# Performance work log

Measured on AMD Instinct MI355X. Metric: run time of the kernel, lower is better.

Reference implementation:

```python
import jax, jax.numpy as jnp
import numpy as np

NCHARS = 50000
NWORDS = 500000
NIC = 64      # ninput_char
NIW = 64      # ninput_word
NH = 128      # nhidden
NA = 5        # naction (nmapping_fn)
B = 65536     # batch size


def setup_inputs() -> dict:
    key = jax.random.key(0)
    ks = jax.random.split(key, 12)
    s = 0.05
    return {
        "x": jax.random.randint(ks[0], (B, 2), 0, NCHARS),
        "y": jax.random.randint(ks[1], (B,), 0, NWORDS),
        "cemb_table": jax.random.normal(ks[2], (NCHARS, NIC), jnp.float32) * s,
        "wemb_table": jax.random.normal(ks[3], (NWORDS, NIW), jnp.float32) * s,
        # Policy MLP: Linear(2*NIC -> NH), ReLU, Linear(NH -> NA), Softmax
        "Wp1": jax.random.normal(ks[4], (2 * NIC, NH), jnp.float32) * s,
        "bp1": jnp.zeros((NH,), jnp.float32),
        "Wp2": jax.random.normal(ks[5], (NH, NA), jnp.float32) * s,
        "bp2": jnp.zeros((NA,), jnp.float32),
        # NA expert MLPs, stacked: Linear(2*NIC -> NH), ReLU, Linear(NH -> NIW)
        "We1": jax.random.normal(ks[6], (NA, 2 * NIC, NH), jnp.float32) * s,
        "be1": jnp.zeros((NA, NH), jnp.float32),
        "We2": jax.random.normal(ks[7], (NA, NH, NIW), jnp.float32) * s,
        "be2": jnp.zeros((NA, NIW), jnp.float32),
    }


def reference(x, y, cemb_table, wemb_table, Wp1, bp1, Wp2, bp2, We1, be1, We2, be2):
    bsize = x.shape[0]
    # char_embs(x).view(bsize, -1): [B, 2*NIC]
    cembs = cemb_table[x].reshape(bsize, -1)

    # Policy (dropout off in eval): probs = softmax(relu(cembs@Wp1+bp1)@Wp2+bp2)
    # Categorical sampling over probs == categorical over the pre-softmax logits.
    logits = jnp.maximum(cembs @ Wp1 + bp1, 0.0) @ Wp2 + bp2
    action = jax.random.categorical(jax.random.key(42), logits)   # [B]
    action_mask = jax.nn.one_hot(action, NA, dtype=cembs.dtype)   # [B, NA]

    # Dense evaluation of all NA experts (matches the Python loop + stack)
    h = jnp.maximum(jnp.einsum('bd,adh->bah', cembs, We1) + be1, 0.0)  # [B, NA, NH]
    mapped = jnp.einsum('bah,aho->bao', h, We2) + be2                  # [B, NA, NIW]

    # sum(unsqueeze(mask,-1) * mapped, dim=1)
    out = jnp.einsum('ba,bao->bo', action_mask, mapped)               # [B, NIW]

    wemb = wemb_table[y]                                              # [B, NIW]
    return (out, wemb)
```

## Files before the change

### kernel.cpp

```cpp
#include <hip/hip_runtime.h>
#include <stdint.h>

#define B_N   65536
#define NIC   64
#define NIW   64
#define NH    128
#define NA    5
#define D2    128

#define PARTITIONABLE 1

#define P2_NCHUNK 51
#define P2_R      1286

typedef __attribute__((ext_vector_type(8))) short short8;
typedef __attribute__((ext_vector_type(4))) float f32x4;

__device__ __forceinline__ ushort f2bf(float f) {
  uint32_t u = __float_as_uint(f);
  uint32_t r = (u + 0x7FFFu + ((u >> 16) & 1u)) >> 16;
  return (ushort)r;
}

__device__ __forceinline__ void split2(float f, ushort& h, ushort& l) {
  h = f2bf(f);
  l = f2bf(f - __uint_as_float(((uint32_t)h) << 16));
}

__device__ __forceinline__ void threefry2x32_k042(uint32_t x0, uint32_t x1,
                                                  uint32_t& o0, uint32_t& o1) {
  const uint32_t ks0 = 0u;
  const uint32_t ks1 = 42u;
  const uint32_t ks2 = 0x1BD11BDAu ^ 0u ^ 42u;
  x0 += ks0; x1 += ks1;
#define TF_RND(r) { x0 += x1; x1 = (x1 << (r)) | (x1 >> (32 - (r))); x1 ^= x0; }
  TF_RND(13) TF_RND(15) TF_RND(26) TF_RND(6)
  x0 += ks1; x1 += ks2 + 1u;
  TF_RND(17) TF_RND(29) TF_RND(16) TF_RND(24)
  x0 += ks2; x1 += ks0 + 2u;
  TF_RND(13) TF_RND(15) TF_RND(26) TF_RND(6)
  x0 += ks0; x1 += ks1 + 3u;
  TF_RND(17) TF_RND(29) TF_RND(16) TF_RND(24)
  x0 += ks1; x1 += ks2 + 4u;
  TF_RND(13) TF_RND(15) TF_RND(26) TF_RND(6)
  x0 += ks2; x1 += ks0 + 5u;
#undef TF_RND
  o0 = x0; o1 = x1;
}

__device__ __forceinline__ float gumbel_at(uint32_t idx) {
  uint32_t bits;
#if PARTITIONABLE
  uint32_t a, b;
  threefry2x32_k042(0u, idx, a, b);
  bits = a ^ b;
#else
  const uint32_t HALF = (uint32_t)(B_N * NA) / 2u;
  uint32_t a, b;
  if (idx < HALF) { threefry2x32_k042(idx, idx + HALF, a, b); bits = a; }
  else            { threefry2x32_k042(idx - HALF, idx, a, b); bits = b; }
#endif
  const float f = __uint_as_float((bits >> 9) | 0x3f800000u) - 1.0f;
  const double u = (f == 0.0f) ? (double)0x1p-126 : (double)f;
  const float nl = (float)(-log(u));
  const float g  = (float)(-log((double)nl));
  return g;
}

__global__ __launch_bounds__(512, 1) void policy_kernel(
    const int* __restrict__ x, const int* __restrict__ y,
    const float* __restrict__ cemb, const float* __restrict__ wemb,
    const float* __restrict__ Wp1, const float* __restrict__ bp1,
    const float* __restrict__ Wp2, const float* __restrict__ bp2,
    float* __restrict__ out_wemb, int* __restrict__ action) {
  __shared__ __align__(16) ushort sW1h[32 * 512];
  __shared__ __align__(16) ushort sW1l[32 * 512];
  __shared__ __align__(16) float sCH[128][132];
  __shared__ __align__(16) float sW2t[NA][NH];
  __shared__ __align__(16) float sb1[NH];
  __shared__ __align__(16) float sScore[128][6];

  const int tid = threadIdx.x;
  const int base = blockIdx.x * 128;

  {
    const int n = tid & 127, q = tid >> 7;
    const int fb = (n >> 4) * 4 + q;
    const int c16 = n & 15;
#pragma unroll
    for (int grp = 0; grp < 4; grp++) {
      short8 ph, pl;
#pragma unroll
      for (int j = 0; j < 8; j++) {
        const int k = 32 * q + 8 * grp + j;
        ushort hh, ll;
        split2(Wp1[k * NH + n], hh, ll);
        ph[j] = (short)hh;
        pl[j] = (short)ll;
      }
      *(short8*)&sW1h[fb * 512 + (c16 + 16 * grp) * 8] = ph;
      *(short8*)&sW1l[fb * 512 + (c16 + 16 * grp) * 8] = pl;
    }
    if (tid < NH) sb1[tid] = bp1[tid];
    if (tid < NA * 32) {
      const int a = tid >> 5, k0 = (tid & 31) * 4;
#pragma unroll
      for (int j = 0; j < 4; j++) sW2t[a][k0 + j] = Wp2[(k0 + j) * NA + a];
    }
  }

  const int wave = tid >> 6, lane = tid & 63;
  const int c16 = lane & 15, h2 = lane >> 4;

  const int grow = base + wave * 16 + c16;
  const int xi0 = x[grow * 2], xi1 = x[grow * 2 + 1];
  short8 Ah[4], Al[4];
#pragma unroll
  for (int kt = 0; kt < 4; kt++) {
    const int xi = (kt < 2) ? xi0 : xi1;
    const float* src = cemb + (size_t)xi * NIC + (kt & 1) * 32 + h2 * 8;
    const float4 aa = *(const float4*)src;
    const float4 bb = *(const float4*)(src + 4);
    ushort hh, ll;
    short8 ph, pl;
    split2(aa.x, hh, ll); ph[0] = (short)hh; pl[0] = (short)ll;
    split2(aa.y, hh, ll); ph[1] = (short)hh; pl[1] = (short)ll;
    split2(aa.z, hh, ll); ph[2] = (short)hh; pl[2] = (short)ll;
    split2(aa.w, hh, ll); ph[3] = (short)hh; pl[3] = (short)ll;
    split2(bb.x, hh, ll); ph[4] = (short)hh; pl[4] = (short)ll;
    split2(bb.y, hh, ll); ph[5] = (short)hh; pl[5] = (short)ll;
    split2(bb.z, hh, ll); ph[6] = (short)hh; pl[6] = (short)ll;
    split2(bb.w, hh, ll); ph[7] = (short)hh; pl[7] = (short)ll;
    Ah[kt] = ph;
    Al[kt] = pl;
  }
  __syncthreads();

  f32x4 acc[8];
#pragma unroll
  for (int ct = 0; ct < 8; ct++) {
    const float bv = sb1[ct * 16 + c16];
    acc[ct] = (f32x4){bv, bv, bv, bv};
  }
#pragma unroll
  for (int kt = 0; kt < 4; kt++) {
#pragma unroll
    for (int ct = 0; ct < 8; ct++) {
      const short8 Bh = *(const short8*)&sW1h[(ct * 4 + kt) * 512 + lane * 8];
      const short8 Bl = *(const short8*)&sW1l[(ct * 4 + kt) * 512 + lane * 8];
      acc[ct] = __builtin_amdgcn_mfma_f32_16x16x32_bf16(Ah[kt], Bh, acc[ct], 0, 0, 0);
      acc[ct] = __builtin_amdgcn_mfma_f32_16x16x32_bf16(Al[kt], Bh, acc[ct], 0, 0, 0);
      acc[ct] = __builtin_amdgcn_mfma_f32_16x16x32_bf16(Ah[kt], Bl, acc[ct], 0, 0, 0);
      acc[ct] = __builtin_amdgcn_mfma_f32_16x16x32_bf16(Al[kt], Bl, acc[ct], 0, 0, 0);
    }
  }
  {
    const int rowb = wave * 16 + h2 * 4;
#pragma unroll
    for (int ct = 0; ct < 8; ct++) {
      const int n = ct * 16 + c16;
#pragma unroll
      for (int r = 0; r < 4; r++)
        sCH[rowb + r][n] = fmaxf(acc[ct][r], 0.0f);
    }
  }
  __syncthreads();

#pragma unroll 1
  for (int p = tid; p < 128 * NA; p += 512) {
    const int row = p / NA, a = p - NA * row;
    float s0 = 0.f, s1 = 0.f, s2 = 0.f, s3 = 0.f;
#pragma unroll 4
    for (int k = 0; k < NH; k += 4) {
      const float4 h4 = *(const float4*)&sCH[row][k];
      const float4 w4 = *(const float4*)&sW2t[a][k];
      s0 = fmaf(h4.x, w4.x, s0);
      s1 = fmaf(h4.y, w4.y, s1);
      s2 = fmaf(h4.z, w4.z, s2);
      s3 = fmaf(h4.w, w4.w, s3);
    }
    const float logit = ((s0 + s1) + (s2 + s3)) + bp2[a];
    sScore[row][a] = gumbel_at((uint32_t)((base + row) * NA + a)) + logit;
  }
  __syncthreads();

  if (tid < 128) {
    int best = 0;
    float bs = sScore[tid][0];
#pragma unroll
    for (int a = 1; a < NA; a++) {
      const float s = sScore[tid][a];
      if (s > bs) { bs = s; best = a; }
    }
    action[base + tid] = best;
  }

#pragma unroll 1
  for (int i = tid; i < 128 * 16; i += 512) {
    const int row = i >> 4, seg = i & 15;
    ((float4*)out_wemb)[(size_t)(base + row) * 16 + seg] =
        ((const float4*)wemb)[(size_t)y[base + row] * 16 + seg];
  }
}

__global__ __launch_bounds__(512, 1) void expert_kernel(
    const int* __restrict__ x, const float* __restrict__ cemb,
    const float* __restrict__ We1, const float* __restrict__ be1,
    const float* __restrict__ We2, const float* __restrict__ be2,
    const int* __restrict__ action, float* __restrict__ out) {
  __shared__ __align__(16) ushort sW1[32 * 512];
  __shared__ __align__(16) ushort sW2[16 * 512];
  __shared__ __align__(16) ushort sCt[8][4 * 512];
  __shared__ __align__(16) ushort sHt[8][4 * 512];
  __shared__ __align__(16) float sbe1[NH];
  __shared__ __align__(16) float sbe2[NIW];
  __shared__ int sList[P2_R];
  __shared__ int sCount;

  const int tid = threadIdx.x;
  const int a = blockIdx.x % NA;
  const int chunk = blockIdx.x / NA;
  const int rowBeg = chunk * P2_R;
  const int rowEnd = (rowBeg + P2_R < B_N) ? rowBeg + P2_R : B_N;

  if (tid == 0) sCount = 0;
  __syncthreads();

  for (int r = rowBeg + tid; r < rowEnd; r += 512)
    if (action[r] == a) sList[atomicAdd(&sCount, 1)] = r;

  {
    const float* W1g = We1 + (size_t)a * D2 * NH;
    const int n = tid & 127, q = tid >> 7;
    const int fb = (n >> 4) * 4 + q;
    const int c16 = n & 15;
#pragma unroll
    for (int grp = 0; grp < 4; grp++) {
      short8 pk;
#pragma unroll
      for (int j = 0; j < 8; j++) {
        const int k = 32 * q + 8 * grp + j;
        pk[j] = (short)f2bf(W1g[k * NH + n]);
      }
      *(short8*)&sW1[fb * 512 + (c16 + 16 * grp) * 8] = pk;
    }
    if (tid < NH) sbe1[tid] = be1[a * NH + tid];
    if (tid < NIW) sbe2[tid] = be2[a * NIW + tid];
  }
  {
    const float* W2g = We2 + (size_t)a * NH * NIW;
    const int o = tid & 63, hq = tid >> 6;
    const int fb = (o >> 4) * 4 + (hq >> 1);
    const int c16 = o & 15;
#pragma unroll
    for (int g2 = 0; g2 < 2; g2++) {
      const int grp = (hq & 1) * 2 + g2;
      short8 pk;
#pragma unroll
      for (int j = 0; j < 8; j++) {
        const int h = 16 * hq + 8 * g2 + j;
        pk[j] = (short)f2bf(W2g[h * NIW + o]);
      }
      *(short8*)&sW2[fb * 512 + (c16 + 16 * grp) * 8] = pk;
    }
  }
  __syncthreads();

  const int cnt = sCount;
  if (cnt == 0) return;

  const int wave = tid >> 6, lane = tid & 63;
  const int rowb = (lane >> 4) * 4;
  ushort* myCt = sCt[wave];
  ushort* myHt = sHt[wave];

#pragma unroll 1
  for (int t16 = wave * 16; t16 < cnt; t16 += 128) {
    {
      const int rt = lane >> 2, q = lane & 3;
      int li = t16 + rt;
      const int g = sList[(li < cnt) ? li : 0];
      const int xi = x[2 * g + (q >> 1)];
      const float4* src = (const float4*)(cemb + (size_t)xi * NIC + (q & 1) * 32);
#pragma unroll
      for (int grp = 0; grp < 4; grp++) {
        const float4 aa = src[2 * grp], bb = src[2 * grp + 1];
        short8 pk;
        pk[0] = (short)f2bf(aa.x); pk[1] = (short)f2bf(aa.y);
        pk[2] = (short)f2bf(aa.z); pk[3] = (short)f2bf(aa.w);
        pk[4] = (short)f2bf(bb.x); pk[5] = (short)f2bf(bb.y);
        pk[6] = (short)f2bf(bb.z); pk[7] = (short)f2bf(bb.w);
        *(short8*)&myCt[q * 512 + (rt + 16 * grp) * 8] = pk;
      }
    }

    short8 A[4];
#pragma unroll
    for (int kt = 0; kt < 4; kt++) A[kt] = *(const short8*)&myCt[kt * 512 + lane * 8];
#pragma unroll
    for (int ct = 0; ct < 8; ct++) {
      const int n = ct * 16 + (lane & 15);
      const float bv = sbe1[n];
      f32x4 acc = {bv, bv, bv, bv};
#pragma unroll
      for (int kt = 0; kt < 4; kt++) {
        const short8 Bf = *(const short8*)&sW1[(ct * 4 + kt) * 512 + lane * 8];
        acc = __builtin_amdgcn_mfma_f32_16x16x32_bf16(A[kt], Bf, acc, 0, 0, 0);
      }
      const int kt2 = n >> 5, grp2 = (n & 31) >> 3, j2 = n & 7;
#pragma unroll
      for (int r = 0; r < 4; r++) {
        const float hv = fmaxf(acc[r], 0.0f);
        myHt[kt2 * 512 + ((rowb + r) + 16 * grp2) * 8 + j2] = f2bf(hv);
      }
    }

    short8 A2[4];
#pragma unroll
    for (int kt = 0; kt < 4; kt++) A2[kt] = *(const short8*)&myHt[kt * 512 + lane * 8];
    int gr4[4];
#pragma unroll
    for (int r = 0; r < 4; r++) {
      const int li2 = t16 + rowb + r;
      gr4[r] = (li2 < cnt) ? sList[li2] : -1;
    }
#pragma unroll
    for (int ot = 0; ot < 4; ot++) {
      const int o = ot * 16 + (lane & 15);
      const float bv = sbe2[o];
      f32x4 o4 = {bv, bv, bv, bv};
#pragma unroll
      for (int kt = 0; kt < 4; kt++) {
        const short8 Bf = *(const short8*)&sW2[(ot * 4 + kt) * 512 + lane * 8];
        o4 = __builtin_amdgcn_mfma_f32_16x16x32_bf16(A2[kt], Bf, o4, 0, 0, 0);
      }
#pragma unroll
      for (int r = 0; r < 4; r++) {
        if (gr4[r] >= 0) out[(size_t)gr4[r] * NIW + o] = o4[r];
      }
    }
  }
}

extern "C" void kernel_launch(void* const* d_in, const int* in_sizes, int n_in,
                              void* d_out, int out_size, void* d_ws, size_t ws_size,
                              hipStream_t stream) {
  const int*   x    = (const int*)d_in[0];
  const int*   y    = (const int*)d_in[1];
  const float* cemb = (const float*)d_in[2];
  const float* wemb = (const float*)d_in[3];
  const float* Wp1  = (const float*)d_in[4];
  const float* bp1  = (const float*)d_in[5];
  const float* Wp2  = (const float*)d_in[6];
  const float* bp2  = (const float*)d_in[7];
  const float* We1  = (const float*)d_in[8];
  const float* be1  = (const float*)d_in[9];
  const float* We2  = (const float*)d_in[10];
  const float* be2  = (const float*)d_in[11];

  float* out      = (float*)d_out;
  float* out_wemb = out + (size_t)B_N * NIW;
  int*   action   = (int*)d_ws;

  policy_kernel<<<B_N / 128, 512, 0, stream>>>(
      x, y, cemb, wemb, Wp1, bp1, Wp2, bp2, out_wemb, action);
  expert_kernel<<<NA * P2_NCHUNK, 512, 0, stream>>>(
      x, cemb, We1, be1, We2, be2, action, out);
}
```

Baseline: 50.73 us.

## Prepack expert weights in policy launch and gather experts per 128-row block

Five extra blocks in the policy kernel convert the expert weights to bf16 MFMA layout once and store them in the workspace. A new expert kernel then reads those packed weights straight from global memory, so it no longer stages them in LDS. Each block groups its own 128 rows by action and runs 16-row tiles for every expert, with higher occupancy. The policy GEMM also drops the lo*lo split-bf16 MFMA term, trading a little logit precision for fewer MFMAs, which could flip sampled actions near ties.

```diff
diff --git a/kernel.cpp b/kernel.cpp
--- a/kernel.cpp
+++ b/kernel.cpp
@@ -10,8 +10,14 @@
 
 #define PARTITIONABLE 1
 
+#define NBLK  512
+
 #define P2_NCHUNK 51
 #define P2_R      1286
+
+#define WS_ACTION_BYTES  262144
+#define WS_PREP_BYTES    245760
+#define WS_NEED_FAST     (WS_ACTION_BYTES + WS_PREP_BYTES)
 
 typedef __attribute__((ext_vector_type(8))) short short8;
 typedef __attribute__((ext_vector_type(4))) float f32x4;
@@ -72,7 +78,9 @@
     const float* __restrict__ cemb, const float* __restrict__ wemb,
     const float* __restrict__ Wp1, const float* __restrict__ bp1,
     const float* __restrict__ Wp2, const float* __restrict__ bp2,
-    float* __restrict__ out_wemb, int* __restrict__ action) {
+    const float* __restrict__ We1, const float* __restrict__ We2,
+    float* __restrict__ out_wemb, int* __restrict__ action,
+    ushort* __restrict__ wPrep) {
   __shared__ __align__(16) ushort sW1h[32 * 512];
   __shared__ __align__(16) ushort sW1l[32 * 512];
   __shared__ __align__(16) float sCH[128][132];
@@ -81,12 +89,48 @@
   __shared__ __align__(16) float sScore[128][6];
 
   const int tid = threadIdx.x;
+
+  if (blockIdx.x >= NBLK) {
+    const int a = blockIdx.x - NBLK;
+    ushort* wp = wPrep + (size_t)a * 24576;
+    {
+      const float* W1g = We1 + (size_t)a * D2 * NH;
+      const int n = tid & 127, q = tid >> 7;
+      const int fb = (n >> 4) * 4 + q;
+      const int cc = n & 15;
+#pragma unroll
+      for (int grp = 0; grp < 4; grp++) {
+        short8 pk;
+#pragma unroll
+        for (int j = 0; j < 8; j++)
+          pk[j] = (short)f2bf(W1g[(32 * q + 8 * grp + j) * NH + n]);
+        *(short8*)&wp[fb * 512 + (cc + 16 * grp) * 8] = pk;
+      }
+    }
+    {
+      const float* W2g = We2 + (size_t)a * NH * NIW;
+      const int o = tid & 63, hq = tid >> 6;
+      const int fb = (o >> 4) * 4 + (hq >> 1);
+      const int cc = o & 15;
+#pragma unroll
+      for (int g2 = 0; g2 < 2; g2++) {
+        const int grp = (hq & 1) * 2 + g2;
+        short8 pk;
+#pragma unroll
+        for (int j = 0; j < 8; j++)
+          pk[j] = (short)f2bf(W2g[(16 * hq + 8 * g2 + j) * NIW + o]);
+        *(short8*)&wp[16384 + fb * 512 + (cc + 16 * grp) * 8] = pk;
+      }
+    }
+    return;
+  }
+
   const int base = blockIdx.x * 128;
 
   {
     const int n = tid & 127, q = tid >> 7;
     const int fb = (n >> 4) * 4 + q;
-    const int c16 = n & 15;
+    const int cc = n & 15;
 #pragma unroll
     for (int grp = 0; grp < 4; grp++) {
       short8 ph, pl;
@@ -98,8 +142,8 @@
         ph[j] = (short)hh;
         pl[j] = (short)ll;
       }
-      *(short8*)&sW1h[fb * 512 + (c16 + 16 * grp) * 8] = ph;
-      *(short8*)&sW1l[fb * 512 + (c16 + 16 * grp) * 8] = pl;
+      *(short8*)&sW1h[fb * 512 + (cc + 16 * grp) * 8] = ph;
+      *(short8*)&sW1l[fb * 512 + (cc + 16 * grp) * 8] = pl;
     }
     if (tid < NH) sb1[tid] = bp1[tid];
     if (tid < NA * 32) {
@@ -151,7 +195,6 @@
       acc[ct] = __builtin_amdgcn_mfma_f32_16x16x32_bf16(Ah[kt], Bh, acc[ct], 0, 0, 0);
       acc[ct] = __builtin_amdgcn_mfma_f32_16x16x32_bf16(Al[kt], Bh, acc[ct], 0, 0, 0);
       acc[ct] = __builtin_amdgcn_mfma_f32_16x16x32_bf16(Ah[kt], Bl, acc[ct], 0, 0, 0);
-      acc[ct] = __builtin_amdgcn_mfma_f32_16x16x32_bf16(Al[kt], Bl, acc[ct], 0, 0, 0);
     }
   }
   {
@@ -203,7 +246,117 @@
   }
 }
 
-__global__ __launch_bounds__(512, 1) void expert_kernel(
+__global__ __launch_bounds__(512, 4) void expert_prepacked(
+    const int* __restrict__ x, const float* __restrict__ cemb,
+    const float* __restrict__ be1, const float* __restrict__ be2,
+    const int* __restrict__ action, const ushort* __restrict__ wPrep,
+    float* __restrict__ out) {
+  __shared__ __align__(16) ushort sHt[8][2048];
+  __shared__ int sList[NA][128];
+  __shared__ int sCnt[NA];
+  __shared__ __align__(16) float sbe1f[NA * NH];
+  __shared__ __align__(16) float sbe2f[NA * NIW];
+
+  const int tid = threadIdx.x;
+  const int base = blockIdx.x * 128;
+
+  if (tid < NA) sCnt[tid] = 0;
+  __syncthreads();
+  if (tid < 128) {
+    const int a = action[base + tid];
+    const int p = atomicAdd(&sCnt[a], 1);
+    sList[a][p] = base + tid;
+  }
+  for (int i = tid; i < NA * NH; i += 512) sbe1f[i] = be1[i];
+  for (int i = tid; i < NA * NIW; i += 512) sbe2f[i] = be2[i];
+  __syncthreads();
+
+  int cnts[NA], pre[NA + 1];
+  pre[0] = 0;
+#pragma unroll
+  for (int a = 0; a < NA; a++) {
+    cnts[a] = sCnt[a];
+    pre[a + 1] = pre[a] + ((cnts[a] + 15) >> 4);
+  }
+  const int T = pre[NA];
+
+  const int wave = tid >> 6, lane = tid & 63;
+  const int c16 = lane & 15, h2 = lane >> 4;
+  const int rowb = h2 * 4;
+  ushort* myHt = sHt[wave];
+
+#pragma unroll 1
+  for (int t = wave; t < T; t += 8) {
+    int a = 0;
+#pragma unroll
+    for (int q = 1; q < NA; q++) if (t >= pre[q]) a = q;
+    const int ti = t - pre[a];
+    const int cnt = cnts[a];
+    const ushort* wp1 = wPrep + (size_t)a * 24576;
+    const ushort* wp2 = wp1 + 16384;
+
+    const int slot = ti * 16 + c16;
+    const int g = sList[a][(slot < cnt) ? slot : 0];
+    const int2 xi2 = ((const int2*)x)[g];
+    short8 Ah[4];
+#pragma unroll
+    for (int kt = 0; kt < 4; kt++) {
+      const float* src = cemb + (size_t)((kt < 2) ? xi2.x : xi2.y) * NIC +
+                         (kt & 1) * 32 + h2 * 8;
+      const float4 aa = *(const float4*)src;
+      const float4 bb = *(const float4*)(src + 4);
+      short8 pk;
+      pk[0] = (short)f2bf(aa.x); pk[1] = (short)f2bf(aa.y);
+      pk[2] = (short)f2bf(aa.z); pk[3] = (short)f2bf(aa.w);
+      pk[4] = (short)f2bf(bb.x); pk[5] = (short)f2bf(bb.y);
+      pk[6] = (short)f2bf(bb.z); pk[7] = (short)f2bf(bb.w);
+      Ah[kt] = pk;
+    }
+
+#pragma unroll
+    for (int ct = 0; ct < 8; ct++) {
+      const float bv = sbe1f[a * NH + ct * 16 + c16];
+      f32x4 acc = {bv, bv, bv, bv};
+#pragma unroll
+      for (int kt = 0; kt < 4; kt++) {
+        const short8 Bf = *(const short8*)&wp1[(ct * 4 + kt) * 512 + lane * 8];
+        acc = __builtin_amdgcn_mfma_f32_16x16x32_bf16(Ah[kt], Bf, acc, 0, 0, 0);
+      }
+      const int n = ct * 16 + c16;
+      const int kt2 = n >> 5, grp2 = (n & 31) >> 3, j2 = n & 7;
+#pragma unroll
+      for (int r = 0; r < 4; r++)
+        myHt[kt2 * 512 + ((rowb + r) + 16 * grp2) * 8 + j2] =
+            f2bf(fmaxf(acc[r], 0.0f));
+    }
+
+    short8 A2[4];
+#pragma unroll
+    for (int kt = 0; kt < 4; kt++)
+      A2[kt] = *(const short8*)&myHt[kt * 512 + lane * 8];
+    int gr4[4];
+#pragma unroll
+    for (int r = 0; r < 4; r++) {
+      const int li2 = ti * 16 + rowb + r;
+      gr4[r] = (li2 < cnt) ? sList[a][li2] : -1;
+    }
+#pragma unroll
+    for (int ot = 0; ot < 4; ot++) {
+      const float bv = sbe2f[a * NIW + ot * 16 + c16];
+      f32x4 o4 = {bv, bv, bv, bv};
+#pragma unroll
+      for (int kt = 0; kt < 4; kt++) {
+        const short8 Bf = *(const short8*)&wp2[(ot * 4 + kt) * 512 + lane * 8];
+        o4 = __builtin_amdgcn_mfma_f32_16x16x32_bf16(A2[kt], Bf, o4, 0, 0, 0);
+      }
+#pragma unroll
+      for (int r = 0; r < 4; r++)
+        if (gr4[r] >= 0) out[(size_t)gr4[r] * NIW + ot * 16 + c16] = o4[r];
+    }
+  }
+}
+
+__global__ __launch_bounds__(512, 1) void expert_staged(
     const int* __restrict__ x, const float* __restrict__ cemb,
     const float* __restrict__ We1, const float* __restrict__ be1,
     const float* __restrict__ We2, const float* __restrict__ be2,
@@ -233,16 +386,14 @@
     const float* W1g = We1 + (size_t)a * D2 * NH;
     const int n = tid & 127, q = tid >> 7;
     const int fb = (n >> 4) * 4 + q;
-    const int c16 = n & 15;
+    const int cc = n & 15;
 #pragma unroll
     for (int grp = 0; grp < 4; grp++) {
       short8 pk;
 #pragma unroll
-      for (int j = 0; j < 8; j++) {
-        const int k = 32 * q + 8 * grp + j;
-        pk[j] = (short)f2bf(W1g[k * NH + n]);
-      }
-      *(short8*)&sW1[fb * 512 + (c16 + 16 * grp) * 8] = pk;
+      for (int j = 0; j < 8; j++)
+        pk[j] = (short)f2bf(W1g[(32 * q + 8 * grp + j) * NH + n]);
+      *(short8*)&sW1[fb * 512 + (cc + 16 * grp) * 8] = pk;
     }
     if (tid < NH) sbe1[tid] = be1[a * NH + tid];
     if (tid < NIW) sbe2[tid] = be2[a * NIW + tid];
@@ -251,17 +402,15 @@
     const float* W2g = We2 + (size_t)a * NH * NIW;
     const int o = tid & 63, hq = tid >> 6;
     const int fb = (o >> 4) * 4 + (hq >> 1);
-    const int c16 = o & 15;
+    const int cc = o & 15;
 #pragma unroll
     for (int g2 = 0; g2 < 2; g2++) {
       const int grp = (hq & 1) * 2 + g2;
       short8 pk;
 #pragma unroll
-      for (int j = 0; j < 8; j++) {
-        const int h = 16 * hq + 8 * g2 + j;
-        pk[j] = (short)f2bf(W2g[h * NIW + o]);
-      }
-      *(short8*)&sW2[fb * 512 + (c16 + 16 * grp) * 8] = pk;
+      for (int j = 0; j < 8; j++)
+        pk[j] = (short)f2bf(W2g[(16 * hq + 8 * g2 + j) * NIW + o]);
+      *(short8*)&sW2[fb * 512 + (cc + 16 * grp) * 8] = pk;
     }
   }
   __syncthreads();
@@ -309,10 +458,9 @@
       }
       const int kt2 = n >> 5, grp2 = (n & 31) >> 3, j2 = n & 7;
 #pragma unroll
-      for (int r = 0; r < 4; r++) {
-        const float hv = fmaxf(acc[r], 0.0f);
-        myHt[kt2 * 512 + ((rowb + r) + 16 * grp2) * 8 + j2] = f2bf(hv);
-      }
+      for (int r = 0; r < 4; r++)
+        myHt[kt2 * 512 + ((rowb + r) + 16 * grp2) * 8 + j2] =
+            f2bf(fmaxf(acc[r], 0.0f));
     }
 
     short8 A2[4];
@@ -335,9 +483,8 @@
         o4 = __builtin_amdgcn_mfma_f32_16x16x32_bf16(A2[kt], Bf, o4, 0, 0, 0);
       }
 #pragma unroll
-      for (int r = 0; r < 4; r++) {
+      for (int r = 0; r < 4; r++)
         if (gr4[r] >= 0) out[(size_t)gr4[r] * NIW + o] = o4[r];
-      }
     }
   }
 }
@@ -360,10 +507,20 @@
 
   float* out      = (float*)d_out;
   float* out_wemb = out + (size_t)B_N * NIW;
-  int*   action   = (int*)d_ws;
-
-  policy_kernel<<<B_N / 128, 512, 0, stream>>>(
-      x, y, cemb, wemb, Wp1, bp1, Wp2, bp2, out_wemb, action);
-  expert_kernel<<<NA * P2_NCHUNK, 512, 0, stream>>>(
-      x, cemb, We1, be1, We2, be2, action, out);
-}
+  int*    action  = (int*)d_ws;
+  ushort* wPrep   = (ushort*)((char*)d_ws + WS_ACTION_BYTES);
+
+  const bool fast = (ws_size >= (size_t)WS_NEED_FAST);
+
+  if (fast) {
+    policy_kernel<<<NBLK + NA, 512, 0, stream>>>(
+        x, y, cemb, wemb, Wp1, bp1, Wp2, bp2, We1, We2, out_wemb, action, wPrep);
+    expert_prepacked<<<NBLK, 512, 0, stream>>>(
+        x, cemb, be1, be2, action, wPrep, out);
+  } else {
+    policy_kernel<<<NBLK, 512, 0, stream>>>(
+        x, y, cemb, wemb, Wp1, bp1, Wp2, bp2, We1, We2, out_wemb, action, wPrep);
+    expert_staged<<<NA * P2_NCHUNK, 512, 0, stream>>>(
+        x, cemb, We1, be1, We2, be2, action, out);
+  }
+}
```

After: 59.62 us. 17.5% more time.

## Fuse policy and expert kernels with per-block action bucketing and prepacked weights

Applied to the files above, without the earlier changes.

Merges the policy and expert passes into one kernel: each block computes actions for its 128 rows, buckets the rows by action in shared memory, and runs the expert MLPs on those rows while reusing the bf16 char-embedding fragments kept in LDS. A small prepack kernel converts the expert weights to bf16 MFMA layout once, and the fused kernel reads them from global/L2 instead of loading them per block. It also drops the low*low correction MFMA in the policy GEMM. This removes the action round-trip, the second launch and the second embedding gather, at the cost of expert weights being streamed from L2 on every tile and slightly lower precision in the policy logits, which could flip sampled actions.

```diff
diff --git a/kernel.cpp b/kernel.cpp
--- a/kernel.cpp
+++ b/kernel.cpp
@@ -10,8 +10,7 @@
 
 #define PARTITIONABLE 1
 
-#define P2_NCHUNK 51
-#define P2_R      1286
+#define NBLK  512
 
 typedef __attribute__((ext_vector_type(8))) short short8;
 typedef __attribute__((ext_vector_type(4))) float f32x4;
@@ -67,18 +66,61 @@
   return g;
 }
 
-__global__ __launch_bounds__(512, 1) void policy_kernel(
+__global__ __launch_bounds__(512, 1) void prepack_kernel(
+    const float* __restrict__ We1, const float* __restrict__ We2,
+    ushort* __restrict__ wPrep) {
+  const int tid = threadIdx.x;
+  const int a = blockIdx.x;
+  ushort* wp = wPrep + (size_t)a * 24576;
+  {
+    const float* W1g = We1 + (size_t)a * D2 * NH;
+    const int n = tid & 127, q = tid >> 7;
+    const int fb = (n >> 4) * 4 + q;
+    const int cc = n & 15;
+#pragma unroll
+    for (int grp = 0; grp < 4; grp++) {
+      short8 pk;
+#pragma unroll
+      for (int j = 0; j < 8; j++)
+        pk[j] = (short)f2bf(W1g[(32 * q + 8 * grp + j) * NH + n]);
+      *(short8*)&wp[fb * 512 + (cc + 16 * grp) * 8] = pk;
+    }
+  }
+  {
+    const float* W2g = We2 + (size_t)a * NH * NIW;
+    const int o = tid & 63, hq = tid >> 6;
+    const int fb = (o >> 4) * 4 + (hq >> 1);
+    const int cc = o & 15;
+#pragma unroll
+    for (int g2 = 0; g2 < 2; g2++) {
+      const int grp = (hq & 1) * 2 + g2;
+      short8 pk;
+#pragma unroll
+      for (int j = 0; j < 8; j++)
+        pk[j] = (short)f2bf(W2g[(16 * hq + 8 * g2 + j) * NIW + o]);
+      *(short8*)&wp[16384 + fb * 512 + (cc + 16 * grp) * 8] = pk;
+    }
+  }
+}
+
+__global__ __launch_bounds__(512, 1) void fused_kernel(
     const int* __restrict__ x, const int* __restrict__ y,
     const float* __restrict__ cemb, const float* __restrict__ wemb,
     const float* __restrict__ Wp1, const float* __restrict__ bp1,
     const float* __restrict__ Wp2, const float* __restrict__ bp2,
-    float* __restrict__ out_wemb, int* __restrict__ action) {
-  __shared__ __align__(16) ushort sW1h[32 * 512];
-  __shared__ __align__(16) ushort sW1l[32 * 512];
+    const float* __restrict__ be1, const float* __restrict__ be2,
+    const ushort* __restrict__ wPrep,
+    float* __restrict__ out, float* __restrict__ out_wemb) {
+  __shared__ __align__(16) ushort sW1h[16384];
+  __shared__ __align__(16) ushort sW1l[16384];
   __shared__ __align__(16) float sCH[128][132];
   __shared__ __align__(16) float sW2t[NA][NH];
   __shared__ __align__(16) float sb1[NH];
   __shared__ __align__(16) float sScore[128][6];
+  __shared__ __align__(16) float sbe1f[NA * NH];
+  __shared__ __align__(16) float sbe2f[NA * NIW];
+  __shared__ int sList[NA][128];
+  __shared__ int sCnt[NA];
 
   const int tid = threadIdx.x;
   const int base = blockIdx.x * 128;
@@ -86,7 +128,7 @@
   {
     const int n = tid & 127, q = tid >> 7;
     const int fb = (n >> 4) * 4 + q;
-    const int c16 = n & 15;
+    const int cc = n & 15;
 #pragma unroll
     for (int grp = 0; grp < 4; grp++) {
       short8 ph, pl;
@@ -98,8 +140,8 @@
         ph[j] = (short)hh;
         pl[j] = (short)ll;
       }
-      *(short8*)&sW1h[fb * 512 + (c16 + 16 * grp) * 8] = ph;
-      *(short8*)&sW1l[fb * 512 + (c16 + 16 * grp) * 8] = pl;
+      *(short8*)&sW1h[fb * 512 + (cc + 16 * grp) * 8] = ph;
+      *(short8*)&sW1l[fb * 512 + (cc + 16 * grp) * 8] = pl;
     }
     if (tid < NH) sb1[tid] = bp1[tid];
     if (tid < NA * 32) {
@@ -107,12 +149,23 @@
 #pragma unroll
       for (int j = 0; j < 4; j++) sW2t[a][k0 + j] = Wp2[(k0 + j) * NA + a];
     }
+    if (tid < NA) sCnt[tid] = 0;
+  }
+  for (int i = tid; i < NA * NH; i += 512) sbe1f[i] = be1[i];
+  for (int i = tid; i < NA * NIW; i += 512) sbe2f[i] = be2[i];
+
+#pragma unroll 1
+  for (int i = tid; i < 128 * 16; i += 512) {
+    const int row = i >> 4, seg = i & 15;
+    ((float4*)out_wemb)[(size_t)(base + row) * 16 + seg] =
+        ((const float4*)wemb)[(size_t)y[base + row] * 16 + seg];
   }
 
   const int wave = tid >> 6, lane = tid & 63;
   const int c16 = lane & 15, h2 = lane >> 4;
 
-  const int grow = base + wave * 16 + c16;
+  const int rloc = wave * 16 + c16;
+  const int grow = base + rloc;
   const int xi0 = x[grow * 2], xi1 = x[grow * 2 + 1];
   short8 Ah[4], Al[4];
 #pragma unroll
@@ -151,9 +204,11 @@
       acc[ct] = __builtin_amdgcn_mfma_f32_16x16x32_bf16(Ah[kt], Bh, acc[ct], 0, 0, 0);
       acc[ct] = __builtin_amdgcn_mfma_f32_16x16x32_bf16(Al[kt], Bh, acc[ct], 0, 0, 0);
       acc[ct] = __builtin_amdgcn_mfma_f32_16x16x32_bf16(Ah[kt], Bl, acc[ct], 0, 0, 0);
-      acc[ct] = __builtin_amdgcn_mfma_f32_16x16x32_bf16(Al[kt], Bl, acc[ct], 0, 0, 0);
-    }
-  }
+    }
+  }
+  __syncthreads();
+
+  ushort* sAf = sW1h;
   {
     const int rowb = wave * 16 + h2 * 4;
 #pragma unroll
@@ -162,6 +217,11 @@
 #pragma unroll
       for (int r = 0; r < 4; r++)
         sCH[rowb + r][n] = fmaxf(acc[ct][r], 0.0f);
+    }
+#pragma unroll
+    for (int kt = 0; kt < 4; kt++) {
+      const int cs = (kt * 4 + h2 + rloc) & 15;
+      *(short8*)&sAf[rloc * 128 + cs * 8] = Ah[kt];
     }
   }
   __syncthreads();
@@ -192,152 +252,80 @@
       const float s = sScore[tid][a];
       if (s > bs) { bs = s; best = a; }
     }
-    action[base + tid] = best;
-  }
+    const int p = atomicAdd(&sCnt[best], 1);
+    sList[best][p] = tid;
+  }
+  __syncthreads();
+
+  const int c0 = sCnt[0], c1 = sCnt[1], c2 = sCnt[2], c3 = sCnt[3], c4 = sCnt[4];
+  const int p1 = (c0 + 15) >> 4;
+  const int p2 = p1 + ((c1 + 15) >> 4);
+  const int p3 = p2 + ((c2 + 15) >> 4);
+  const int p4 = p3 + ((c3 + 15) >> 4);
+  const int T  = p4 + ((c4 + 15) >> 4);
+
+  const int rowb = h2 * 4;
+  ushort* myHt = sW1l + wave * 2048;
 
 #pragma unroll 1
-  for (int i = tid; i < 128 * 16; i += 512) {
-    const int row = i >> 4, seg = i & 15;
-    ((float4*)out_wemb)[(size_t)(base + row) * 16 + seg] =
-        ((const float4*)wemb)[(size_t)y[base + row] * 16 + seg];
-  }
-}
-
-__global__ __launch_bounds__(512, 1) void expert_kernel(
-    const int* __restrict__ x, const float* __restrict__ cemb,
-    const float* __restrict__ We1, const float* __restrict__ be1,
-    const float* __restrict__ We2, const float* __restrict__ be2,
-    const int* __restrict__ action, float* __restrict__ out) {
-  __shared__ __align__(16) ushort sW1[32 * 512];
-  __shared__ __align__(16) ushort sW2[16 * 512];
-  __shared__ __align__(16) ushort sCt[8][4 * 512];
-  __shared__ __align__(16) ushort sHt[8][4 * 512];
-  __shared__ __align__(16) float sbe1[NH];
-  __shared__ __align__(16) float sbe2[NIW];
-  __shared__ int sList[P2_R];
-  __shared__ int sCount;
-
-  const int tid = threadIdx.x;
-  const int a = blockIdx.x % NA;
-  const int chunk = blockIdx.x / NA;
-  const int rowBeg = chunk * P2_R;
-  const int rowEnd = (rowBeg + P2_R < B_N) ? rowBeg + P2_R : B_N;
-
-  if (tid == 0) sCount = 0;
-  __syncthreads();
-
-  for (int r = rowBeg + tid; r < rowEnd; r += 512)
-    if (action[r] == a) sList[atomicAdd(&sCount, 1)] = r;
-
-  {
-    const float* W1g = We1 + (size_t)a * D2 * NH;
-    const int n = tid & 127, q = tid >> 7;
-    const int fb = (n >> 4) * 4 + q;
-    const int c16 = n & 15;
-#pragma unroll
-    for (int grp = 0; grp < 4; grp++) {
-      short8 pk;
-#pragma unroll
-      for (int j = 0; j < 8; j++) {
-        const int k = 32 * q + 8 * grp + j;
-        pk[j] = (short)f2bf(W1g[k * NH + n]);
+  for (int t = wave; t < T; t += 8) {
+    int a = 0, ti = t, cnt = c0;
+    if (t >= p1) { a = 1; ti = t - p1; cnt = c1; }
+    if (t >= p2) { a = 2; ti = t - p2; cnt = c2; }
+    if (t >= p3) { a = 3; ti = t - p3; cnt = c3; }
+    if (t >= p4) { a = 4; ti = t - p4; cnt = c4; }
+    const ushort* wp1 = wPrep + (size_t)a * 24576;
+    const ushort* wp2 = wp1 + 16384;
+
+    const int slot = ti * 16 + c16;
+    const int rl = sList[a][(slot < cnt) ? slot : 0];
+    short8 Ae[4];
+#pragma unroll
+    for (int kt = 0; kt < 4; kt++) {
+      const int cs = (kt * 4 + h2 + rl) & 15;
+      Ae[kt] = *(const short8*)&sAf[rl * 128 + cs * 8];
+    }
+
+#pragma unroll
+    for (int ct = 0; ct < 8; ct++) {
+      const float bv = sbe1f[a * NH + ct * 16 + c16];
+      f32x4 ac = {bv, bv, bv, bv};
+#pragma unroll
+      for (int kt = 0; kt < 4; kt++) {
+        const short8 Bf = *(const short8*)&wp1[(ct * 4 + kt) * 512 + lane * 8];
+        ac = __builtin_amdgcn_mfma_f32_16x16x32_bf16(Ae[kt], Bf, ac, 0, 0, 0);
       }
-      *(short8*)&sW1[fb * 512 + (c16 + 16 * grp) * 8] = pk;
-    }
-    if (tid < NH) sbe1[tid] = be1[a * NH + tid];
-    if (tid < NIW) sbe2[tid] = be2[a * NIW + tid];
-  }
-  {
-    const float* W2g = We2 + (size_t)a * NH * NIW;
-    const int o = tid & 63, hq = tid >> 6;
-    const int fb = (o >> 4) * 4 + (hq >> 1);
-    const int c16 = o & 15;
-#pragma unroll
-    for (int g2 = 0; g2 < 2; g2++) {
-      const int grp = (hq & 1) * 2 + g2;
-      short8 pk;
-#pragma unroll
-      for (int j = 0; j < 8; j++) {
-        const int h = 16 * hq + 8 * g2 + j;
-        pk[j] = (short)f2bf(W2g[h * NIW + o]);
-      }
-      *(short8*)&sW2[fb * 512 + (c16 + 16 * grp) * 8] = pk;
-    }
-  }
-  __syncthreads();
-
-  const int cnt = sCount;
-  if (cnt == 0) return;
-
-  const int wave = tid >> 6, lane = tid & 63;
-  const int rowb = (lane >> 4) * 4;
-  ushort* myCt = sCt[wave];
-  ushort* myHt = sHt[wave];
-
-#pragma unroll 1
-  for (int t16 = wave * 16; t16 < cnt; t16 += 128) {
-    {
-      const int rt = lane >> 2, q = lane & 3;
-      int li = t16 + rt;
-      const int g = sList[(li < cnt) ? li : 0];
-      const int xi = x[2 * g + (q >> 1)];
-      const float4* src = (const float4*)(cemb + (size_t)xi * NIC + (q & 1) * 32);
-#pragma unroll
-      for (int grp = 0; grp < 4; grp++) {
-        const float4 aa = src[2 * grp], bb = src[2 * grp + 1];
-        short8 pk;
-        pk[0] = (short)f2bf(aa.x); pk[1] = (short)f2bf(aa.y);
-        pk[2] = (short)f2bf(aa.z); pk[3] = (short)f2bf(aa.w);
-        pk[4] = (short)f2bf(bb.x); pk[5] = (short)f2bf(bb.y);
-        pk[6] = (short)f2bf(bb.z); pk[7] = (short)f2bf(bb.w);
-        *(short8*)&myCt[q * 512 + (rt + 16 * grp) * 8] = pk;
-      }
-    }
-
-    short8 A[4];
-#pragma unroll
-    for (int kt = 0; kt < 4; kt++) A[kt] = *(const short8*)&myCt[kt * 512 + lane * 8];
-#pragma unroll
-    for (int ct = 0; ct < 8; ct++) {
-      const int n = ct * 16 + (lane & 15);
-      const float bv = sbe1[n];
-      f32x4 acc = {bv, bv, bv, bv};
+      const int n = ct * 16 + c16;
+      const int kt2 = n >> 5, grp2 = (n & 31) >> 3, j2 = n & 7;
+#pragma unroll
+      for (int r = 0; r < 4; r++)
+        myHt[kt2 * 512 + ((rowb + r) + 16 * grp2) * 8 + j2] =
+            f2bf(fmaxf(ac[r], 0.0f));
+    }
+
+    short8 A2[4];
+#pragma unroll
+    for (int kt = 0; kt < 4; kt++)
+      A2[kt] = *(const short8*)&myHt[kt * 512 + lane * 8];
+    int gr4[4];
+#pragma unroll
+    for (int r = 0; r < 4; r++) {
+      const int li2 = ti * 16 + rowb + r;
+      gr4[r] = (li2 < cnt) ? sList[a][li2] : -1;
+    }
+#pragma unroll
+    for (int ot = 0; ot < 4; ot++) {
+      const float bv = sbe2f[a * NIW + ot * 16 + c16];
+      f32x4 o4 = {bv, bv, bv, bv};
 #pragma unroll
       for (int kt = 0; kt < 4; kt++) {
-        const short8 Bf = *(const short8*)&sW1[(ct * 4 + kt) * 512 + lane * 8];
-        acc = __builtin_amdgcn_mfma_f32_16x16x32_bf16(A[kt], Bf, acc, 0, 0, 0);
-      }
-      const int kt2 = n >> 5, grp2 = (n & 31) >> 3, j2 = n & 7;
-#pragma unroll
-      for (int r = 0; r < 4; r++) {
-        const float hv = fmaxf(acc[r], 0.0f);
-        myHt[kt2 * 512 + ((rowb + r) + 16 * grp2) * 8 + j2] = f2bf(hv);
-      }
-    }
-
-    short8 A2[4];
-#pragma unroll
-    for (int kt = 0; kt < 4; kt++) A2[kt] = *(const short8*)&myHt[kt * 512 + lane * 8];
-    int gr4[4];
-#pragma unroll
-    for (int r = 0; r < 4; r++) {
-      const int li2 = t16 + rowb + r;
-      gr4[r] = (li2 < cnt) ? sList[li2] : -1;
-    }
-#pragma unroll
-    for (int ot = 0; ot < 4; ot++) {
-      const int o = ot * 16 + (lane & 15);
-      const float bv = sbe2[o];
-      f32x4 o4 = {bv, bv, bv, bv};
-#pragma unroll
-      for (int kt = 0; kt < 4; kt++) {
-        const short8 Bf = *(const short8*)&sW2[(ot * 4 + kt) * 512 + lane * 8];
+        const short8 Bf = *(const short8*)&wp2[(ot * 4 + kt) * 512 + lane * 8];
         o4 = __builtin_amdgcn_mfma_f32_16x16x32_bf16(A2[kt], Bf, o4, 0, 0, 0);
       }
 #pragma unroll
-      for (int r = 0; r < 4; r++) {
-        if (gr4[r] >= 0) out[(size_t)gr4[r] * NIW + o] = o4[r];
-      }
+      for (int r = 0; r < 4; r++)
+        if (gr4[r] >= 0)
+          out[(size_t)(base + gr4[r]) * NIW + ot * 16 + c16] = o4[r];
     }
   }
 }
@@ -360,10 +348,9 @@
 
   float* out      = (float*)d_out;
   float* out_wemb = out + (size_t)B_N * NIW;
-  int*   action   = (int*)d_ws;
-
-  policy_kernel<<<B_N / 128, 512, 0, stream>>>(
-      x, y, cemb, wemb, Wp1, bp1, Wp2, bp2, out_wemb, action);
-  expert_kernel<<<NA * P2_NCHUNK, 512, 0, stream>>>(
-      x, cemb, We1, be1, We2, be2, action, out);
-}
+  ushort* wPrep   = (ushort*)d_ws;
+
+  prepack_kernel<<<NA, 512, 0, stream>>>(We1, We2, wPrep);
+  fused_kernel<<<NBLK, 512, 0, stream>>>(
+      x, y, cemb, wemb, Wp1, bp1, Wp2, bp2, be1, be2, wPrep, out, out_wemb);
+}
```

Measured after the change: 55.75 us. 9.9% more time.

## Fuse policy second layer into registers and drop low-low MFMA term

Applied to the files above, without the earlier changes.

The policy kernel now computes the second linear layer directly from the MFMA accumulators, using per-lane partial sums reduced with wave shuffles, then does the Gumbel argmax via shuffles. This removes the sCH and sScore shared buffers and two block barriers. The layer-1 accumulation is split into two halves to lower register pressure, and launch bounds are raised so more blocks fit per CU. The Al*Bl split-bf16 MFMA term is dropped, which slightly reduces policy precision and could flip near-tie action choices.

```diff
diff --git a/kernel.cpp b/kernel.cpp
--- a/kernel.cpp
+++ b/kernel.cpp
@@ -67,18 +67,17 @@
   return g;
 }
 
-__global__ __launch_bounds__(512, 1) void policy_kernel(
+__global__ __launch_bounds__(512, 4) void policy_kernel(
     const int* __restrict__ x, const int* __restrict__ y,
     const float* __restrict__ cemb, const float* __restrict__ wemb,
     const float* __restrict__ Wp1, const float* __restrict__ bp1,
     const float* __restrict__ Wp2, const float* __restrict__ bp2,
     float* __restrict__ out_wemb, int* __restrict__ action) {
-  __shared__ __align__(16) ushort sW1h[32 * 512];
-  __shared__ __align__(16) ushort sW1l[32 * 512];
-  __shared__ __align__(16) float sCH[128][132];
+  __shared__ __align__(16) ushort sW1h[16384];
+  __shared__ __align__(16) ushort sW1l[16384];
   __shared__ __align__(16) float sW2t[NA][NH];
   __shared__ __align__(16) float sb1[NH];
-  __shared__ __align__(16) float sScore[128][6];
+  __shared__ __align__(16) float sbp2[8];
 
   const int tid = threadIdx.x;
   const int base = blockIdx.x * 128;
@@ -86,7 +85,7 @@
   {
     const int n = tid & 127, q = tid >> 7;
     const int fb = (n >> 4) * 4 + q;
-    const int c16 = n & 15;
+    const int cc = n & 15;
 #pragma unroll
     for (int grp = 0; grp < 4; grp++) {
       short8 ph, pl;
@@ -98,8 +97,8 @@
         ph[j] = (short)hh;
         pl[j] = (short)ll;
       }
-      *(short8*)&sW1h[fb * 512 + (c16 + 16 * grp) * 8] = ph;
-      *(short8*)&sW1l[fb * 512 + (c16 + 16 * grp) * 8] = pl;
+      *(short8*)&sW1h[fb * 512 + (cc + 16 * grp) * 8] = ph;
+      *(short8*)&sW1l[fb * 512 + (cc + 16 * grp) * 8] = pl;
     }
     if (tid < NH) sb1[tid] = bp1[tid];
     if (tid < NA * 32) {
@@ -107,6 +106,7 @@
 #pragma unroll
       for (int j = 0; j < 4; j++) sW2t[a][k0 + j] = Wp2[(k0 + j) * NA + a];
     }
+    if (tid < NA) sbp2[tid] = bp2[tid];
   }
 
   const int wave = tid >> 6, lane = tid & 63;
@@ -136,64 +136,93 @@
   }
   __syncthreads();
 
-  f32x4 acc[8];
-#pragma unroll
-  for (int ct = 0; ct < 8; ct++) {
-    const float bv = sb1[ct * 16 + c16];
-    acc[ct] = (f32x4){bv, bv, bv, bv};
-  }
-#pragma unroll
-  for (int kt = 0; kt < 4; kt++) {
-#pragma unroll
-    for (int ct = 0; ct < 8; ct++) {
-      const short8 Bh = *(const short8*)&sW1h[(ct * 4 + kt) * 512 + lane * 8];
-      const short8 Bl = *(const short8*)&sW1l[(ct * 4 + kt) * 512 + lane * 8];
-      acc[ct] = __builtin_amdgcn_mfma_f32_16x16x32_bf16(Ah[kt], Bh, acc[ct], 0, 0, 0);
-      acc[ct] = __builtin_amdgcn_mfma_f32_16x16x32_bf16(Al[kt], Bh, acc[ct], 0, 0, 0);
-      acc[ct] = __builtin_amdgcn_mfma_f32_16x16x32_bf16(Ah[kt], Bl, acc[ct], 0, 0, 0);
-      acc[ct] = __builtin_amdgcn_mfma_f32_16x16x32_bf16(Al[kt], Bl, acc[ct], 0, 0, 0);
-    }
-  }
-  {
-    const int rowb = wave * 16 + h2 * 4;
-#pragma unroll
-    for (int ct = 0; ct < 8; ct++) {
-      const int n = ct * 16 + c16;
-#pragma unroll
-      for (int r = 0; r < 4; r++)
-        sCH[rowb + r][n] = fmaxf(acc[ct][r], 0.0f);
-    }
-  }
-  __syncthreads();
-
-#pragma unroll 1
-  for (int p = tid; p < 128 * NA; p += 512) {
-    const int row = p / NA, a = p - NA * row;
-    float s0 = 0.f, s1 = 0.f, s2 = 0.f, s3 = 0.f;
-#pragma unroll 4
-    for (int k = 0; k < NH; k += 4) {
-      const float4 h4 = *(const float4*)&sCH[row][k];
-      const float4 w4 = *(const float4*)&sW2t[a][k];
-      s0 = fmaf(h4.x, w4.x, s0);
-      s1 = fmaf(h4.y, w4.y, s1);
-      s2 = fmaf(h4.z, w4.z, s2);
-      s3 = fmaf(h4.w, w4.w, s3);
-    }
-    const float logit = ((s0 + s1) + (s2 + s3)) + bp2[a];
-    sScore[row][a] = gumbel_at((uint32_t)((base + row) * NA + a)) + logit;
-  }
-  __syncthreads();
-
-  if (tid < 128) {
-    int best = 0;
-    float bs = sScore[tid][0];
-#pragma unroll
-    for (int a = 1; a < NA; a++) {
-      const float s = sScore[tid][a];
-      if (s > bs) { bs = s; best = a; }
-    }
-    action[base + tid] = best;
-  }
+  float part[4][5];
+#pragma unroll
+  for (int r = 0; r < 4; r++)
+#pragma unroll
+    for (int a = 0; a < NA; a++) part[r][a] = 0.0f;
+
+#pragma unroll
+  for (int half = 0; half < 2; half++) {
+    f32x4 acc[4];
+#pragma unroll
+    for (int c2 = 0; c2 < 4; c2++) {
+      const float bv = sb1[(half * 4 + c2) * 16 + c16];
+      acc[c2] = (f32x4){bv, bv, bv, bv};
+    }
+#pragma unroll
+    for (int kt = 0; kt < 4; kt++) {
+#pragma unroll
+      for (int c2 = 0; c2 < 4; c2++) {
+        const int fb = (half * 4 + c2) * 4 + kt;
+        const short8 Bh = *(const short8*)&sW1h[fb * 512 + lane * 8];
+        const short8 Bl = *(const short8*)&sW1l[fb * 512 + lane * 8];
+        acc[c2] = __builtin_amdgcn_mfma_f32_16x16x32_bf16(Ah[kt], Bh, acc[c2], 0, 0, 0);
+        acc[c2] = __builtin_amdgcn_mfma_f32_16x16x32_bf16(Al[kt], Bh, acc[c2], 0, 0, 0);
+        acc[c2] = __builtin_amdgcn_mfma_f32_16x16x32_bf16(Ah[kt], Bl, acc[c2], 0, 0, 0);
+      }
+    }
+#pragma unroll
+    for (int c2 = 0; c2 < 4; c2++) {
+      const int ct = half * 4 + c2;
+      float w[NA];
+#pragma unroll
+      for (int a = 0; a < NA; a++) w[a] = sW2t[a][ct * 16 + c16];
+#pragma unroll
+      for (int r = 0; r < 4; r++) {
+        const float hv = fmaxf(acc[c2][r], 0.0f);
+#pragma unroll
+        for (int a = 0; a < NA; a++) part[r][a] = fmaf(hv, w[a], part[r][a]);
+      }
+    }
+  }
+
+#pragma unroll
+  for (int st = 1; st <= 8; st <<= 1) {
+#pragma unroll
+    for (int r = 0; r < 4; r++)
+#pragma unroll
+      for (int a = 0; a < NA; a++)
+        part[r][a] += __shfl_xor(part[r][a], st);
+  }
+
+  float score0, score1;
+  {
+    const int r0_ = c16 / 5, a0_ = c16 - 5 * (c16 / 5);
+    float lg = 0.0f;
+#pragma unroll
+    for (int r = 0; r < 4; r++)
+#pragma unroll
+      for (int a = 0; a < NA; a++)
+        if (r0_ == r && a0_ == a) lg = part[r][a];
+    const float logit = lg + sbp2[a0_];
+    const int growr = base + wave * 16 + h2 * 4 + r0_;
+    score0 = gumbel_at((uint32_t)(growr * NA + a0_)) + logit;
+  }
+  {
+    const int a1_ = (c16 & 3) + 1;
+    float lg = 0.0f;
+#pragma unroll
+    for (int a = 1; a < NA; a++)
+      if (a1_ == a) lg = part[3][a];
+    const float logit = lg + sbp2[a1_];
+    const int growr = base + wave * 16 + h2 * 4 + 3;
+    score1 = gumbel_at((uint32_t)(growr * NA + a1_)) + logit;
+  }
+
+  int best = 0;
+  float bs = 0.0f;
+#pragma unroll
+  for (int a = 0; a < NA; a++) {
+    const int idx = c16 * 5 + a;
+    const int src = h2 * 16 + ((idx < 16) ? idx : (idx - 16));
+    const float v0 = __shfl(score0, src);
+    const float v1 = __shfl(score1, src);
+    const float s = (idx < 16) ? v0 : v1;
+    if (a == 0) bs = s;
+    else if (s > bs) { bs = s; best = a; }
+  }
+  if (c16 < 4) action[base + wave * 16 + h2 * 4 + c16] = best;
 
 #pragma unroll 1
   for (int i = tid; i < 128 * 16; i += 512) {
@@ -203,7 +232,7 @@
   }
 }
 
-__global__ __launch_bounds__(512, 1) void expert_kernel(
+__global__ __launch_bounds__(512, 1) void expert_staged(
     const int* __restrict__ x, const float* __restrict__ cemb,
     const float* __restrict__ We1, const float* __restrict__ be1,
     const float* __restrict__ We2, const float* __restrict__ be2,
@@ -233,16 +262,14 @@
     const float* W1g = We1 + (size_t)a * D2 * NH;
     const int n = tid & 127, q = tid >> 7;
     const int fb = (n >> 4) * 4 + q;
-    const int c16 = n & 15;
+    const int cc = n & 15;
 #pragma unroll
     for (int grp = 0; grp < 4; grp++) {
       short8 pk;
 #pragma unroll
-      for (int j = 0; j < 8; j++) {
-        const int k = 32 * q + 8 * grp + j;
-        pk[j] = (short)f2bf(W1g[k * NH + n]);
-      }
-      *(short8*)&sW1[fb * 512 + (c16 + 16 * grp) * 8] = pk;
+      for (int j = 0; j < 8; j++)
+        pk[j] = (short)f2bf(W1g[(32 * q + 8 * grp + j) * NH + n]);
+      *(short8*)&sW1[fb * 512 + (cc + 16 * grp) * 8] = pk;
     }
     if (tid < NH) sbe1[tid] = be1[a * NH + tid];
     if (tid < NIW) sbe2[tid] = be2[a * NIW + tid];
@@ -251,17 +278,15 @@
     const float* W2g = We2 + (size_t)a * NH * NIW;
     const int o = tid & 63, hq = tid >> 6;
     const int fb = (o >> 4) * 4 + (hq >> 1);
-    const int c16 = o & 15;
+    const int cc = o & 15;
 #pragma unroll
     for (int g2 = 0; g2 < 2; g2++) {
       const int grp = (hq & 1) * 2 + g2;
       short8 pk;
 #pragma unroll
-      for (int j = 0; j < 8; j++) {
-        const int h = 16 * hq + 8 * g2 + j;
-        pk[j] = (short)f2bf(W2g[h * NIW + o]);
-      }
-      *(short8*)&sW2[fb * 512 + (c16 + 16 * grp) * 8] = pk;
+      for (int j = 0; j < 8; j++)
+        pk[j] = (short)f2bf(W2g[(16 * hq + 8 * g2 + j) * NIW + o]);
+      *(short8*)&sW2[fb * 512 + (cc + 16 * grp) * 8] = pk;
     }
   }
   __syncthreads();
@@ -309,10 +334,9 @@
       }
       const int kt2 = n >> 5, grp2 = (n & 31) >> 3, j2 = n & 7;
 #pragma unroll
-      for (int r = 0; r < 4; r++) {
-        const float hv = fmaxf(acc[r], 0.0f);
-        myHt[kt2 * 512 + ((rowb + r) + 16 * grp2) * 8 + j2] = f2bf(hv);
-      }
+      for (int r = 0; r < 4; r++)
+        myHt[kt2 * 512 + ((rowb + r) + 16 * grp2) * 8 + j2] =
+            f2bf(fmaxf(acc[r], 0.0f));
     }
 
     short8 A2[4];
@@ -335,9 +359,8 @@
         o4 = __builtin_amdgcn_mfma_f32_16x16x32_bf16(A2[kt], Bf, o4, 0, 0, 0);
       }
 #pragma unroll
-      for (int r = 0; r < 4; r++) {
+      for (int r = 0; r < 4; r++)
         if (gr4[r] >= 0) out[(size_t)gr4[r] * NIW + o] = o4[r];
-      }
     }
   }
 }
@@ -364,6 +387,6 @@
 
   policy_kernel<<<B_N / 128, 512, 0, stream>>>(
       x, y, cemb, wemb, Wp1, bp1, Wp2, bp2, out_wemb, action);
-  expert_kernel<<<NA * P2_NCHUNK, 512, 0, stream>>>(
+  expert_staged<<<NA * P2_NCHUNK, 512, 0, stream>>>(
       x, cemb, We1, be1, We2, be2, action, out);
 }
```

After: 42.35 us. 1.2x faster.
